# Kernel optimization log

Hardware: AMD Instinct MI355X
Metric: run time of the kernel (lower is better)

The kernel has to match this reference:

```python
import jax, jax.numpy as jnp
import numpy as np

C = 10.0
EMBEDDING_DIM = 128


def setup_inputs() -> dict:
    key = jax.random.key(0)
    k1, k2 = jax.random.split(key)
    B, P, D, N = 128, 128, 128, 4096
    mh_attn_out = jax.random.normal(k1, (B, P, D), dtype=jnp.float32)
    single_head_key = jax.random.normal(k2, (B, D, N), dtype=jnp.float32)
    mask = jnp.zeros((B, P, N), dtype=jnp.float32)  # additive mask (0 or -inf)
    return {"mh_attn_out": mh_attn_out, "single_head_key": single_head_key, "mask": mask}


def reference(mh_attn_out, single_head_key, mask):
    # score: [B, P, N]
    score = jnp.einsum('bpd,bdn->bpn', mh_attn_out, single_head_key)
    score_scaled = score / jnp.sqrt(jnp.float32(EMBEDDING_DIM))
    score_clipped = C * jnp.tanh(score_scaled)
    score_masked = score_clipped + mask
    probs = jax.nn.softmax(score_masked, axis=-1)
    return probs
```

## Files before the change

kernel.cpp:

```cpp
#include <hip/hip_runtime.h>
#include <math.h>

constexpr int BB = 128;
constexpr int PP = 128;
constexpr int DD = 128;
constexpr int NN = 4096;
constexpr float kC = 10.0f;
constexpr float k2InvSqrtD = 0.1767766952966369f;

constexpr int NTHR = 512;
constexpr int LSTR = 132;

typedef float f32x4 __attribute__((ext_vector_type(4)));
typedef _Float16 f16x4 __attribute__((ext_vector_type(4)));
typedef _Float16 f16x8 __attribute__((ext_vector_type(8)));

__device__ __forceinline__ void st_nt_f4(float* p, float4 s) {
    f32x4 v = {s.x, s.y, s.z, s.w};
    __builtin_nontemporal_store(v, (f32x4*)p);
}

__device__ __forceinline__ float clip1(float s, float m) {
    const float e2 = __expf(s * k2InvSqrtD);
    const float r = __builtin_amdgcn_rcpf(e2 + 1.0f);
    return fmaf(-2.0f * kC, r, kC) + m;
}

__global__ __launch_bounds__(NTHR, 2)
void score_kernel(const float* __restrict__ A,
                  const float* __restrict__ K,
                  const float* __restrict__ M,
                  float* __restrict__ O,
                  float* __restrict__ ws) {
    __shared__ _Float16 Khi[128 * LSTR];
    __shared__ _Float16 Klo[128 * LSTR];

    const int l = blockIdx.x;
    const int b = l >> 5;
    const int ntb = l & 31;
    const int n_base = ntb * 128;

    const int tid = (int)threadIdx.x;
    const int lane = tid & 63;
    const int wid = tid >> 6;
    const int col = lane & 15;
    const int g = lane >> 4;
    const int kbase = 4 * g;

    const float* Kg = K + (size_t)b * DD * NN + n_base;
    #pragma unroll
    for (int i = 0; i < 8; ++i) {
        const int f = tid + i * NTHR;
        const int d = f >> 5;
        const int n4 = (f & 31) << 2;
        const float4 v = *(const float4*)(Kg + (size_t)d * NN + n4);
        const float xs[4] = {v.x, v.y, v.z, v.w};
        #pragma unroll
        for (int e = 0; e < 4; ++e) {
            const float x = xs[e];
            const _Float16 h = (_Float16)x;
            Khi[(n4 + e) * LSTR + d] = h;
            Klo[(n4 + e) * LSTR + d] = (_Float16)(x - (float)h);
        }
    }

    const float* Arow = A + (size_t)(b * PP + wid * 16 + col) * DD;
    f16x8 ah[4], al[4];
    #pragma unroll
    for (int kb = 0; kb < 4; ++kb) {
        #pragma unroll
        for (int j = 0; j < 8; ++j) {
            const int d = kb * 32 + kbase + (j & 3) + 16 * (j >> 2);
            const float x = Arow[d];
            const _Float16 h = (_Float16)x;
            ah[kb][j] = h;
            al[kb][j] = (_Float16)(x - (float)h);
        }
    }
    __syncthreads();

    const size_t mrow0 = (size_t)(b * PP + wid * 16 + kbase) * NN + n_base + col;

    float rsum[4] = {0.f, 0.f, 0.f, 0.f};
    float mv[4];
    #pragma unroll
    for (int j = 0; j < 4; ++j) mv[j] = M[mrow0 + (size_t)j * NN];

    #pragma unroll 2
    for (int nt = 0; nt < 8; ++nt) {
        float mvn[4];
        if (nt < 7) {
            #pragma unroll
            for (int j = 0; j < 4; ++j)
                mvn[j] = M[mrow0 + (size_t)j * NN + (nt + 1) * 16];
        }

        const int nrow = (nt * 16 + col) * LSTR;
        f32x4 acc = {0.f, 0.f, 0.f, 0.f};
        #pragma unroll
        for (int kb = 0; kb < 4; ++kb) {
            const int d0 = kb * 32 + kbase;
            const f16x4 h0 = *(const f16x4*)&Khi[nrow + d0];
            const f16x4 h1 = *(const f16x4*)&Khi[nrow + d0 + 16];
            const f16x4 l0 = *(const f16x4*)&Klo[nrow + d0];
            const f16x4 l1 = *(const f16x4*)&Klo[nrow + d0 + 16];
            const f16x8 bh = __builtin_shufflevector(h0, h1, 0, 1, 2, 3, 4, 5, 6, 7);
            const f16x8 bl = __builtin_shufflevector(l0, l1, 0, 1, 2, 3, 4, 5, 6, 7);
            acc = __builtin_amdgcn_mfma_f32_16x16x32_f16(ah[kb], bh, acc, 0, 0, 0);
            acc = __builtin_amdgcn_mfma_f32_16x16x32_f16(ah[kb], bl, acc, 0, 0, 0);
            acc = __builtin_amdgcn_mfma_f32_16x16x32_f16(al[kb], bh, acc, 0, 0, 0);
        }

        #pragma unroll
        for (int j = 0; j < 4; ++j) {
            const size_t off = mrow0 + (size_t)j * NN + nt * 16;
            const float e = __expf(clip1(acc[j], mv[j]));
            O[off] = e;
            rsum[j] += e;
        }
        #pragma unroll
        for (int j = 0; j < 4; ++j) mv[j] = mvn[j];
    }

    #pragma unroll
    for (int j = 0; j < 4; ++j) {
        float s = rsum[j];
        s += __shfl_xor(s, 1);
        s += __shfl_xor(s, 2);
        s += __shfl_xor(s, 4);
        s += __shfl_xor(s, 8);
        rsum[j] = s;
    }
    if (col == 0) {
        #pragma unroll
        for (int j = 0; j < 4; ++j)
            ws[(size_t)(b * PP + wid * 16 + kbase + j) * 32 + ntb] = rsum[j];
    }
}

__global__ __launch_bounds__(256, 4)
void scale_kernel(float* __restrict__ O, const float* __restrict__ ws) {
    const int gtid = blockIdx.x * 256 + (int)threadIdx.x;
    const int row = gtid >> 5;
    const int seg = gtid & 31;

    const float* w = ws + (size_t)row * 32;
    float s = 0.f;
    #pragma unroll
    for (int i = 0; i < 8; ++i) {
        const float4 v = *(const float4*)(w + i * 4);
        s += (v.x + v.y) + (v.z + v.w);
    }
    const float inv = __builtin_amdgcn_rcpf(s);

    float4* R = (float4*)(O + (size_t)row * NN);
    #pragma unroll 8
    for (int i = 0; i < 32; ++i) {
        const int idx = i * 32 + seg;
        float4 v = R[idx];
        v.x *= inv; v.y *= inv; v.z *= inv; v.w *= inv;
        st_nt_f4((float*)&R[idx], v);
    }
}

extern "C" void kernel_launch(void* const* d_in, const int* in_sizes, int n_in,
                              void* d_out, int out_size, void* d_ws, size_t ws_size,
                              hipStream_t stream) {
    const float* A = (const float*)d_in[0];
    const float* K = (const float*)d_in[1];
    const float* M = (const float*)d_in[2];
    float* O = (float*)d_out;
    float* ws = (float*)d_ws;

    score_kernel<<<dim3(BB * 32), dim3(NTHR), 0, stream>>>(A, K, M, O, ws);
    scale_kernel<<<dim3(2048), dim3(256), 0, stream>>>(O, ws);
}
```

Before: 287.3 us.

## Interleave hi/lo fp16 K tiles into swizzled LDS layout for 128-bit fragment reads

Merges the separate hi and lo fp16 shared-memory tiles of K into one array. Each MFMA B-fragment's 8 halves now sit contiguously in a 16-byte granule, and granule positions are rotated to spread LDS banks. The inner loop issues two 128-bit LDS reads per k-block instead of four 64-bit reads plus shuffles. The staging writes use more complex index arithmetic, and the rotation has to match between writer and reader threads to stay correct.

After: 286.0 us. Within noise of the previous version (-0.5%).

```diff
diff --git a/kernel.cpp b/kernel.cpp
--- a/kernel.cpp
+++ b/kernel.cpp
@@ -9,10 +9,9 @@
 constexpr float k2InvSqrtD = 0.1767766952966369f;
 
 constexpr int NTHR = 512;
-constexpr int LSTR = 132;
+constexpr int RS = 264;
 
 typedef float f32x4 __attribute__((ext_vector_type(4)));
-typedef _Float16 f16x4 __attribute__((ext_vector_type(4)));
 typedef _Float16 f16x8 __attribute__((ext_vector_type(8)));
 
 __device__ __forceinline__ void st_nt_f4(float* p, float4 s) {
@@ -32,8 +31,7 @@
                   const float* __restrict__ M,
                   float* __restrict__ O,
                   float* __restrict__ ws) {
-    __shared__ _Float16 Khi[128 * LSTR];
-    __shared__ _Float16 Klo[128 * LSTR];
+    __shared__ _Float16 Kf[128 * RS];
 
     const int l = blockIdx.x;
     const int b = l >> 5;
@@ -48,19 +46,29 @@
     const int kbase = 4 * g;
 
     const float* Kg = K + (size_t)b * DD * NN + n_base;
-    #pragma unroll
-    for (int i = 0; i < 8; ++i) {
-        const int f = tid + i * NTHR;
-        const int d = f >> 5;
-        const int n4 = (f & 31) << 2;
-        const float4 v = *(const float4*)(Kg + (size_t)d * NN + n4);
-        const float xs[4] = {v.x, v.y, v.z, v.w};
+    {
+        const int d0 = tid >> 5;
+        const int tn = (tid & 31) * 4;
+        const int rotw = tid & 3;
         #pragma unroll
-        for (int e = 0; e < 4; ++e) {
-            const float x = xs[e];
-            const _Float16 h = (_Float16)x;
-            Khi[(n4 + e) * LSTR + d] = h;
-            Klo[(n4 + e) * LSTR + d] = (_Float16)(x - (float)h);
+        for (int i = 0; i < 8; ++i) {
+            const int d = d0 + 16 * i;
+            const int kb = d >> 5;
+            const int dk = d & 31;
+            const int gw = (dk & 15) >> 2;
+            const int j = (dk & 3) + 4 * (dk >> 4);
+            const int granh = kb * 8 + ((2 * gw + rotw) & 7);
+            const int granl = kb * 8 + ((2 * gw + 1 + rotw) & 7);
+            const float4 v = *(const float4*)(Kg + (size_t)d * NN + tn);
+            const float xs[4] = {v.x, v.y, v.z, v.w};
+            #pragma unroll
+            for (int e = 0; e < 4; ++e) {
+                const float x = xs[e];
+                const _Float16 h = (_Float16)x;
+                const int base = (tn + e) * RS;
+                Kf[base + granh * 8 + j] = h;
+                Kf[base + granl * 8 + j] = (_Float16)(x - (float)h);
+            }
         }
     }
 
@@ -75,6 +83,16 @@
             const _Float16 h = (_Float16)x;
             ah[kb][j] = h;
             al[kb][j] = (_Float16)(x - (float)h);
+        }
+    }
+
+    int offH[4], offL[4];
+    {
+        const int rotr = (col >> 2) & 3;
+        #pragma unroll
+        for (int kb = 0; kb < 4; ++kb) {
+            offH[kb] = kb * 64 + ((2 * g + rotr) & 7) * 8;
+            offL[kb] = kb * 64 + ((2 * g + 1 + rotr) & 7) * 8;
         }
     }
     __syncthreads();
@@ -95,17 +113,12 @@
                 mvn[j] = M[mrow0 + (size_t)j * NN + (nt + 1) * 16];
         }
 
-        const int nrow = (nt * 16 + col) * LSTR;
+        const _Float16* Krow = &Kf[(nt * 16 + col) * RS];
         f32x4 acc = {0.f, 0.f, 0.f, 0.f};
         #pragma unroll
         for (int kb = 0; kb < 4; ++kb) {
-            const int d0 = kb * 32 + kbase;
-            const f16x4 h0 = *(const f16x4*)&Khi[nrow + d0];
-            const f16x4 h1 = *(const f16x4*)&Khi[nrow + d0 + 16];
-            const f16x4 l0 = *(const f16x4*)&Klo[nrow + d0];
-            const f16x4 l1 = *(const f16x4*)&Klo[nrow + d0 + 16];
-            const f16x8 bh = __builtin_shufflevector(h0, h1, 0, 1, 2, 3, 4, 5, 6, 7);
-            const f16x8 bl = __builtin_shufflevector(l0, l1, 0, 1, 2, 3, 4, 5, 6, 7);
+            const f16x8 bh = *(const f16x8*)(Krow + offH[kb]);
+            const f16x8 bl = *(const f16x8*)(Krow + offL[kb]);
             acc = __builtin_amdgcn_mfma_f32_16x16x32_f16(ah[kb], bh, acc, 0, 0, 0);
             acc = __builtin_amdgcn_mfma_f32_16x16x32_f16(ah[kb], bl, acc, 0, 0, 0);
             acc = __builtin_amdgcn_mfma_f32_16x16x32_f16(al[kb], bh, acc, 0, 0, 0);
```

## Store K tile in natural n-major layout and read with LDS transpose loads

Applied to the files above, without the earlier changes.

The K tile is now written to shared memory in its natural d-major order with vectorized 8-byte stores, replacing the scalar transposed stores of the old layout. The MFMA B-operand is then fetched with ds_read_b64_tr_b16, which transposes during the read. The goal is to cut the LDS write cost and bank conflicts in the staging phase. In exchange there is an explicit lgkmcnt wait and a sched barrier per tile, which may limit overlap between LDS reads and MFMA.

Result: no change. 287.8 us (+0.2%).

```diff
diff --git a/kernel.cpp b/kernel.cpp
--- a/kernel.cpp
+++ b/kernel.cpp
@@ -9,7 +9,7 @@
 constexpr float k2InvSqrtD = 0.1767766952966369f;
 
 constexpr int NTHR = 512;
-constexpr int LSTR = 132;
+constexpr int TEL = 272;
 
 typedef float f32x4 __attribute__((ext_vector_type(4)));
 typedef _Float16 f16x4 __attribute__((ext_vector_type(4)));
@@ -18,6 +18,12 @@
 __device__ __forceinline__ void st_nt_f4(float* p, float4 s) {
     f32x4 v = {s.x, s.y, s.z, s.w};
     __builtin_nontemporal_store(v, (f32x4*)p);
+}
+
+__device__ __forceinline__ f16x4 tr_read(unsigned addr) {
+    f16x4 r;
+    asm volatile("ds_read_b64_tr_b16 %0, %1" : "=v"(r) : "v"(addr));
+    return r;
 }
 
 __device__ __forceinline__ float clip1(float s, float m) {
@@ -32,8 +38,8 @@
                   const float* __restrict__ M,
                   float* __restrict__ O,
                   float* __restrict__ ws) {
-    __shared__ _Float16 Khi[128 * LSTR];
-    __shared__ _Float16 Klo[128 * LSTR];
+    __shared__ _Float16 Khi[64 * TEL];
+    __shared__ _Float16 Klo[64 * TEL];
 
     const int l = blockIdx.x;
     const int b = l >> 5;
@@ -48,19 +54,25 @@
     const int kbase = 4 * g;
 
     const float* Kg = K + (size_t)b * DD * NN + n_base;
-    #pragma unroll
-    for (int i = 0; i < 8; ++i) {
-        const int f = tid + i * NTHR;
-        const int d = f >> 5;
-        const int n4 = (f & 31) << 2;
-        const float4 v = *(const float4*)(Kg + (size_t)d * NN + n4);
-        const float xs[4] = {v.x, v.y, v.z, v.w};
+    {
+        const int dl = tid >> 5;
+        const int n4 = (tid & 31) * 4;
+        const int tb = n4 >> 4;
+        const int nin = n4 & 12;
         #pragma unroll
-        for (int e = 0; e < 4; ++e) {
-            const float x = xs[e];
-            const _Float16 h = (_Float16)x;
-            Khi[(n4 + e) * LSTR + d] = h;
-            Klo[(n4 + e) * LSTR + d] = (_Float16)(x - (float)h);
+        for (int i = 0; i < 8; ++i) {
+            const float4 v = *(const float4*)(Kg + (size_t)(16 * i + dl) * NN + n4);
+            const float xs[4] = {v.x, v.y, v.z, v.w};
+            f16x4 h, lo;
+            #pragma unroll
+            for (int e = 0; e < 4; ++e) {
+                const _Float16 hh = (_Float16)xs[e];
+                h[e] = hh;
+                lo[e] = (_Float16)(xs[e] - (float)hh);
+            }
+            const int el = (i * 8 + tb) * TEL + dl * 16 + nin;
+            *(f16x4*)&Khi[el] = h;
+            *(f16x4*)&Klo[el] = lo;
         }
     }
 
@@ -79,6 +91,9 @@
     }
     __syncthreads();
 
+    const unsigned khi0 = (unsigned)(uintptr_t)&Khi[0] + (unsigned)lane * 8u;
+    const unsigned klo0 = (unsigned)(uintptr_t)&Klo[0] + (unsigned)lane * 8u;
+
     const size_t mrow0 = (size_t)(b * PP + wid * 16 + kbase) * NN + n_base + col;
 
     float rsum[4] = {0.f, 0.f, 0.f, 0.f};
@@ -88,24 +103,30 @@
 
     #pragma unroll 2
     for (int nt = 0; nt < 8; ++nt) {
-        float mvn[4];
+        float mvn[4] = {0.f, 0.f, 0.f, 0.f};
         if (nt < 7) {
             #pragma unroll
             for (int j = 0; j < 4; ++j)
                 mvn[j] = M[mrow0 + (size_t)j * NN + (nt + 1) * 16];
         }
 
-        const int nrow = (nt * 16 + col) * LSTR;
+        f16x4 bh0[4], bh1[4], bl0[4], bl1[4];
+        #pragma unroll
+        for (int kb = 0; kb < 4; ++kb) {
+            const unsigned t0 = (unsigned)(((2 * kb) * 8 + nt) * (TEL * 2));
+            bh0[kb] = tr_read(khi0 + t0);
+            bh1[kb] = tr_read(khi0 + t0 + 8u * (TEL * 2));
+            bl0[kb] = tr_read(klo0 + t0);
+            bl1[kb] = tr_read(klo0 + t0 + 8u * (TEL * 2));
+        }
+        asm volatile("s_waitcnt lgkmcnt(0)" ::: "memory");
+        __builtin_amdgcn_sched_barrier(0);
+
         f32x4 acc = {0.f, 0.f, 0.f, 0.f};
         #pragma unroll
         for (int kb = 0; kb < 4; ++kb) {
-            const int d0 = kb * 32 + kbase;
-            const f16x4 h0 = *(const f16x4*)&Khi[nrow + d0];
-            const f16x4 h1 = *(const f16x4*)&Khi[nrow + d0 + 16];
-            const f16x4 l0 = *(const f16x4*)&Klo[nrow + d0];
-            const f16x4 l1 = *(const f16x4*)&Klo[nrow + d0 + 16];
-            const f16x8 bh = __builtin_shufflevector(h0, h1, 0, 1, 2, 3, 4, 5, 6, 7);
-            const f16x8 bl = __builtin_shufflevector(l0, l1, 0, 1, 2, 3, 4, 5, 6, 7);
+            const f16x8 bh = __builtin_shufflevector(bh0[kb], bh1[kb], 0, 1, 2, 3, 4, 5, 6, 7);
+            const f16x8 bl = __builtin_shufflevector(bl0[kb], bl1[kb], 0, 1, 2, 3, 4, 5, 6, 7);
             acc = __builtin_amdgcn_mfma_f32_16x16x32_f16(ah[kb], bh, acc, 0, 0, 0);
             acc = __builtin_amdgcn_mfma_f32_16x16x32_f16(ah[kb], bl, acc, 0, 0, 0);
             acc = __builtin_amdgcn_mfma_f32_16x16x32_f16(al[kb], bh, acc, 0, 0, 0);
```
